# Kernel tuning notes

Hardware: AMD Instinct MI355X
Metric: run time of the kernel (lower is better)

The kernel has to match this reference:

```python
import jax, jax.numpy as jnp
import numpy as np

HIDDEN = 1024
HEADS = 16
HEAD_DIM = HIDDEN // HEADS


def setup_inputs() -> dict:
    key = jax.random.key(0)
    k1, k2, k3, k4 = jax.random.split(key, 4)
    x = jax.random.normal(k1, (4, 2048, HIDDEN), dtype=jnp.float32)
    # qkv: Linear(hidden, 3*hidden, bias=False) -> weight [3*hidden, hidden]
    w_qkv = jax.random.normal(k2, (3 * HIDDEN, HIDDEN), dtype=jnp.float32) * (HIDDEN ** -0.5)
    # out_proj: Linear(hidden, hidden) with bias
    w_out = jax.random.normal(k3, (HIDDEN, HIDDEN), dtype=jnp.float32) * (HIDDEN ** -0.5)
    b_out = jax.random.normal(k4, (HIDDEN,), dtype=jnp.float32) * 0.01
    return {"x": x, "w_qkv": w_qkv, "w_out": w_out, "b_out": b_out}


def reference(x, w_qkv, w_out, b_out):
    B, N, _ = x.shape
    scale = HEAD_DIM ** -0.5
    qkv = jnp.einsum('bnc,dc->bnd', x, w_qkv)            # [B,N,3*hidden]
    qkv = qkv.reshape(B, N, 3, HEADS, HEAD_DIM)
    qkv = jnp.transpose(qkv, (2, 0, 3, 1, 4))            # [3,B,H,N,hd]
    q, k, v = qkv[0], qkv[1], qkv[2]
    att = jnp.einsum('bhxd,bhyd->bhxy', q, k) * scale    # [B,H,N,N]
    att = jax.nn.softmax(att, axis=-1)
    out = jnp.einsum('bhxy,bhyd->bhxd', att, v)          # [B,H,N,hd]
    out = jnp.transpose(out, (0, 2, 1, 3)).reshape(B, N, HIDDEN)
    out = jnp.einsum('bnc,dc->bnd', out, w_out) + b_out
    return out
```

## Files before the change

kernel.cpp:

```cpp
#include <hip/hip_runtime.h>

typedef unsigned short u16;
typedef short short8 __attribute__((ext_vector_type(8)));
typedef float f32x4 __attribute__((ext_vector_type(4)));
typedef float f32x16 __attribute__((ext_vector_type(16)));
typedef unsigned short u16x4 __attribute__((ext_vector_type(4)));
typedef unsigned int u32x4 __attribute__((ext_vector_type(4)));

#define MFMA16(a, b, c) __builtin_amdgcn_mfma_f32_16x16x32_bf16((a), (b), (c), 0, 0, 0)
#define MFMA32(a, b, c) __builtin_amdgcn_mfma_f32_32x32x16_bf16((a), (b), (c), 0, 0, 0)

#if __has_builtin(__builtin_amdgcn_exp2f)
#define EXP2F(x) __builtin_amdgcn_exp2f(x)
#else
#define EXP2F(x) exp2f(x)
#endif

__device__ __forceinline__ u16 f2bf(float f) {
    unsigned u = __builtin_bit_cast(unsigned, f);
    u += 0x7FFFu + ((u >> 16) & 1u);
    return (u16)(u >> 16);
}

__device__ __forceinline__ void async16(void* lds, const void* g) {
    __builtin_amdgcn_global_load_lds(
        (const __attribute__((address_space(1))) void*)g,
        (__attribute__((address_space(3))) void*)lds, 16, 0, 0);
}

__device__ __forceinline__ unsigned cvtpk(float lo, float hi) {
    unsigned r;
    asm("v_cvt_pk_bf16_f32 %0, %1, %2" : "=v"(r) : "v"(lo), "v"(hi));
    return r;
}
__device__ __forceinline__ void plswap(unsigned& a, unsigned& b) {
    asm("v_permlane32_swap_b32 %0, %1" : "+v"(a), "+v"(b));
}

__device__ __forceinline__ void packP(const f32x16& s, short8& f0, short8& f1) {
    u32x4 u0, u1;
    {
        unsigned a = cvtpk(s[0], s[1]), b = cvtpk(s[4], s[5]);
        plswap(a, b);
        unsigned c = cvtpk(s[2], s[3]), d = cvtpk(s[6], s[7]);
        plswap(c, d);
        u0[0] = a; u0[1] = c; u0[2] = b; u0[3] = d;
    }
    {
        unsigned a = cvtpk(s[8], s[9]), b = cvtpk(s[12], s[13]);
        plswap(a, b);
        unsigned c = cvtpk(s[10], s[11]), d = cvtpk(s[14], s[15]);
        plswap(c, d);
        u1[0] = a; u1[1] = c; u1[2] = b; u1[3] = d;
    }
    f0 = __builtin_bit_cast(short8, u0);
    f1 = __builtin_bit_cast(short8, u1);
}

__global__ __launch_bounds__(256) void cast3(const float* __restrict__ x,
                                             const float* __restrict__ wqkv,
                                             const float* __restrict__ wout,
                                             u16* __restrict__ dst) {
    const int blk = blockIdx.x;
    const float* src;
    int idx;
    float sc = 1.0f;
    u16* out;
    if (blk < 8192) {
        src = x; out = dst; idx = (blk * 256 + threadIdx.x) * 4;
    } else if (blk < 11264) {
        src = wqkv; out = dst + (size_t)8192 * 1024;
        idx = ((blk - 8192) * 256 + threadIdx.x) * 4;
        if (idx < 1024 * 1024) sc = 0.18033688011112042f;
    } else {
        src = wout; out = dst + (size_t)11264 * 1024;
        idx = ((blk - 11264) * 256 + threadIdx.x) * 4;
    }
    float4 v = *(const float4*)(src + idx);
    u16x4 r;
    r[0] = f2bf(v.x * sc); r[1] = f2bf(v.y * sc);
    r[2] = f2bf(v.z * sc); r[3] = f2bf(v.w * sc);
    *(u16x4*)(out + idx) = r;
}

template <int MODE>
__global__ __launch_bounds__(256, 2) void gemm_bt(const u16* __restrict__ A,
                                                  const u16* __restrict__ B,
                                                  void* __restrict__ C0,
                                                  void* __restrict__ C1,
                                                  int M, int N, int K) {
    __shared__ u16 As[128 * 32];
    __shared__ u16 Bs[128 * 32];
    const int tid = threadIdx.x;
    const int w = tid >> 6, l = tid & 63;
    const int g = l >> 4, lo = l & 15;
    const int mtiles = M >> 7;
    const int tm = blockIdx.x % mtiles, tn = blockIdx.x / mtiles;
    const int rowBase = tm << 7, colBase = tn << 7;
    const int wrow = w >> 1, wcol = w & 1;

    f32x4 acc[4][4] = {};

    const int srow = l >> 2;
    const int scol = (l & 3) * 8;
    const int nk = K >> 5;
    for (int kt = 0; kt < nk; ++kt) {
        const int kbase = kt * 32 + scol;
#pragma unroll
        for (int it = 0; it < 2; ++it) {
            const int seg = it * 4 + w;
            const int r = seg * 16 + srow;
            async16(&As[seg * 512], &A[(size_t)(rowBase + r) * K + kbase]);
            async16(&Bs[seg * 512], &B[(size_t)(colBase + r) * K + kbase]);
        }
        __syncthreads();
        short8 af[4], bf[4];
#pragma unroll
        for (int mi = 0; mi < 4; ++mi)
            af[mi] = *(const short8*)&As[(wrow * 64 + mi * 16 + lo) * 32 + g * 8];
#pragma unroll
        for (int ni = 0; ni < 4; ++ni)
            bf[ni] = *(const short8*)&Bs[(wcol * 64 + ni * 16 + lo) * 32 + g * 8];
#pragma unroll
        for (int mi = 0; mi < 4; ++mi)
#pragma unroll
            for (int ni = 0; ni < 4; ++ni)
                acc[mi][ni] = MFMA16(af[mi], bf[ni], acc[mi][ni]);
        __syncthreads();
    }

    if constexpr (MODE == 0) {
        if (colBase < 2048) {
            u16* qk = (u16*)C0;
#pragma unroll
            for (int ni = 0; ni < 4; ++ni) {
                const int c = colBase + wcol * 64 + ni * 16 + lo;
#pragma unroll
                for (int mi = 0; mi < 4; ++mi) {
                    const int r0 = rowBase + wrow * 64 + mi * 16 + g * 4;
#pragma unroll
                    for (int i = 0; i < 4; ++i)
                        qk[(size_t)(r0 + i) * 2048 + c] = f2bf(acc[mi][ni][i]);
                }
            }
        } else {
            u16* vt = (u16*)C1;
            const int b = rowBase >> 11;
#pragma unroll
            for (int ni = 0; ni < 4; ++ni) {
                const int c = colBase + wcol * 64 + ni * 16 + lo;
                const int hh = (c - 2048) >> 6, d = (c - 2048) & 63;
                u16* vrow = vt + ((size_t)((b * 16 + hh) * 64 + d)) * 2048;
#pragma unroll
                for (int mi = 0; mi < 4; ++mi) {
                    const int r0 = rowBase + wrow * 64 + mi * 16 + g * 4;
                    u16x4 pk;
#pragma unroll
                    for (int i = 0; i < 4; ++i) pk[i] = f2bf(acc[mi][ni][i]);
                    *(u16x4*)(vrow + (r0 & 2047)) = pk;
                }
            }
        }
    } else {
        float* Cf = (float*)C0;
        const float* bias = (const float*)C1;
#pragma unroll
        for (int ni = 0; ni < 4; ++ni) {
            const int c = colBase + wcol * 64 + ni * 16 + lo;
            const float bv = bias[c];
#pragma unroll
            for (int mi = 0; mi < 4; ++mi) {
                const int r0 = rowBase + wrow * 64 + mi * 16 + g * 4;
#pragma unroll
                for (int i = 0; i < 4; ++i)
                    Cf[(size_t)(r0 + i) * N + c] = acc[mi][ni][i] + bv;
            }
        }
    }
}

__global__ __launch_bounds__(256, 4) void attn_fwd(const u16* __restrict__ qkb,
                                                   const u16* __restrict__ vtg,
                                                   u16* __restrict__ outb) {
    __shared__ u16 Ks[2][64 * 64];
    __shared__ u16 Vs[2][64 * 64];
    const int tid = threadIdx.x;
    const int w = tid >> 6, l = tid & 63;
    const int hi = l >> 5, lq = l & 31;

    const int lin = (blockIdx.x & 7) * 128 + (blockIdx.x >> 3);
    const int bh = lin >> 4, qt = lin & 15;
    const int b = bh >> 4, h = bh & 15;
    const size_t rowQ = (size_t)b * 2048 + qt * 128 + w * 32;

    short8 qf[4];
#pragma unroll
    for (int ks = 0; ks < 4; ++ks)
        qf[ks] = *(const short8*)(qkb + (rowQ + lq) * 2048 + h * 64 + ks * 16 + hi * 8);

    int koff[4];
#pragma unroll
    for (int ks = 0; ks < 4; ++ks)
        koff[ks] = (lq * 128 + ks * 32 + hi * 16) ^ ((lq & 7) << 4);

    const int L0 = tid * 16, L1 = tid * 16 + 4096;
    const int kr0 = L0 >> 7, kc0 = ((L0 ^ ((kr0 & 7) << 4)) & 127) >> 1;
    const int kr1 = L1 >> 7, kc1 = ((L1 ^ ((kr1 & 7) << 4)) & 127) >> 1;
    const u16* ks0 = qkb + (size_t)(b * 2048 + kr0) * 2048 + 1024 + h * 64 + kc0;
    const u16* ks1 = qkb + (size_t)(b * 2048 + kr1) * 2048 + 1024 + h * 64 + kc1;
    const u16* vs0 = vtg + ((size_t)bh * 64 + kr0) * 2048 + kc0;
    const u16* vs1 = vtg + ((size_t)bh * 64 + kr1) * 2048 + kc1;
    const size_t KADV = (size_t)64 * 2048;

    f32x16 O0, O1, Ol;
#pragma unroll
    for (int i = 0; i < 16; ++i) { O0[i] = 0.f; O1[i] = 0.f; Ol[i] = 0.f; }
    const f32x16 Z = {};
    const short8 onesv = {16256, 16256, 16256, 16256, 16256, 16256, 16256, 16256};

    async16((char*)Ks[0] + L0, ks0); async16((char*)Ks[0] + L1, ks1);
    async16((char*)Vs[0] + L0, vs0); async16((char*)Vs[0] + L1, vs1);
    ks0 += KADV; ks1 += KADV; vs0 += 64; vs1 += 64;

    int cur = 0;
    for (int kt = 0; kt < 32; ++kt) {
        __syncthreads();
        if (kt < 31) {
            const int nx = cur ^ 1;
            async16((char*)Ks[nx] + L0, ks0); async16((char*)Ks[nx] + L1, ks1);
            async16((char*)Vs[nx] + L0, vs0); async16((char*)Vs[nx] + L1, vs1);
            ks0 += KADV; ks1 += KADV; vs0 += 64; vs1 += 64;
        }
        const char* kb = (const char*)Ks[cur];
        const char* vb = (const char*)Vs[cur];

#pragma unroll
        for (int t = 0; t < 2; ++t) {
            const int tb = t * 4096;
            __builtin_amdgcn_s_setprio(1);
            f32x16 s = MFMA32(*(const short8*)(kb + koff[0] + tb), qf[0], Z);
            s = MFMA32(*(const short8*)(kb + koff[1] + tb), qf[1], s);
            s = MFMA32(*(const short8*)(kb + koff[2] + tb), qf[2], s);
            s = MFMA32(*(const short8*)(kb + koff[3] + tb), qf[3], s);
            __builtin_amdgcn_s_setprio(0);

#pragma unroll
            for (int i = 0; i < 16; ++i) s[i] = EXP2F(s[i]);

            short8 p0, p1;
            packP(s, p0, p1);

            __builtin_amdgcn_s_setprio(1);
            Ol = MFMA32(p0, onesv, Ol);
            Ol = MFMA32(p1, onesv, Ol);
            O0 = MFMA32(p0, *(const short8*)(vb + koff[t * 2]), O0);
            O1 = MFMA32(p0, *(const short8*)(vb + koff[t * 2] + 4096), O1);
            O0 = MFMA32(p1, *(const short8*)(vb + koff[t * 2 + 1]), O0);
            O1 = MFMA32(p1, *(const short8*)(vb + koff[t * 2 + 1] + 4096), O1);
            __builtin_amdgcn_s_setprio(0);
        }
        cur ^= 1;
    }

#pragma unroll
    for (int r = 0; r < 16; ++r) {
        const int qrow = (r & 3) + 8 * (r >> 2) + 4 * hi;
        const float linv = 1.0f / Ol[r];
        u16* op = outb + (rowQ + qrow) * 1024 + h * 64 + lq;
        op[0] = f2bf(O0[r] * linv);
        op[32] = f2bf(O1[r] * linv);
    }
}

extern "C" void kernel_launch(void* const* d_in, const int* in_sizes, int n_in,
                              void* d_out, int out_size, void* d_ws, size_t ws_size,
                              hipStream_t stream) {
    const float* x     = (const float*)d_in[0];
    const float* w_qkv = (const float*)d_in[1];
    const float* w_out = (const float*)d_in[2];
    const float* b_out = (const float*)d_in[3];
    float* out = (float*)d_out;

    u16* xb    = (u16*)d_ws;
    u16* wqkvb = xb    + (size_t)8192 * 1024;
    u16* woutb = wqkvb + (size_t)3072 * 1024;
    u16* qkb   = woutb + (size_t)1024 * 1024;
    u16* vtg   = qkb   + (size_t)8192 * 2048;
    u16* attb  = vtg   + (size_t)64 * 64 * 2048;

    cast3<<<12288, 256, 0, stream>>>(x, w_qkv, w_out, xb);

    gemm_bt<0><<<dim3((8192 / 128) * (3072 / 128)), 256, 0, stream>>>(
        xb, wqkvb, qkb, vtg, 8192, 3072, 1024);

    attn_fwd<<<1024, 256, 0, stream>>>(qkb, vtg, attb);

    gemm_bt<1><<<dim3((8192 / 128) * (1024 / 128)), 256, 0, stream>>>(
        attb, woutb, out, (void*)b_out, 8192, 1024, 1024);
}
```

Before: 187.9 us.

## Replace QKV projection GEMM with 256x256-tile double-buffered swizzled kernel

The QKV projection now runs in a new 512-thread kernel that computes 256x256 output tiles with a 64-wide K step. It double-buffers global-to-LDS async loads, uses an XOR-swizzled LDS layout to avoid bank conflicts, and raises wave priority around the MFMA bursts. The goal is more data reuse per loaded byte and overlap of loads with matrix math, replacing the 128x128, single-buffered, 32-wide-K kernel. In exchange it uses more registers and 128KB of LDS, and launches only 384 blocks, which may hurt occupancy and load balance. The output projection keeps the old kernel, now specialised to the bias mode only.

New measurement: 187.0 us. No clear change (-0.5%).

```diff
diff --git a/kernel.cpp b/kernel.cpp
--- a/kernel.cpp
+++ b/kernel.cpp
@@ -83,11 +83,127 @@
     *(u16x4*)(out + idx) = r;
 }
 
-template <int MODE>
+__global__ __launch_bounds__(512, 2) void gemm256(const u16* __restrict__ A,
+                                                  const u16* __restrict__ B,
+                                                  u16* __restrict__ qk,
+                                                  u16* __restrict__ vt) {
+    __shared__ u16 lds[2][2][16384];
+    const int tid = threadIdx.x;
+    const int l = tid & 63;
+    const int w = tid >> 6;
+    const int g = l >> 4, lo = l & 15;
+    const int wrow = w >> 2, wcol = w & 3;
+    const int tm = blockIdx.x & 31, tn = blockIdx.x >> 5;
+    const int rowBase = tm << 8, colBase = tn << 8;
+
+    const int srow = tid >> 3;
+    const int scol = (((tid * 16) ^ (((tid >> 3) & 7) << 4)) & 127) >> 1;
+    const u16* pa = A + (size_t)(rowBase + srow) * 1024 + scol;
+    const u16* pb = B + (size_t)(colBase + srow) * 1024 + scol;
+    const int ldsOff = tid * 16;
+
+    int abase[2], bbase[2];
+#pragma unroll
+    for (int k = 0; k < 2; ++k) {
+        abase[k] = (((wrow * 128 + lo) * 128 + k * 64 + g * 16) ^ ((lo & 7) << 4));
+        bbase[k] = (((wcol * 64 + lo) * 128 + k * 64 + g * 16) ^ ((lo & 7) << 4));
+    }
+
+    f32x4 acc[8][4] = {};
+
+#define STAGE256(buf, kt)                                                                   \
+    {                                                                                       \
+        const u16* sa = pa + (kt) * 64;                                                     \
+        const u16* sb = pb + (kt) * 64;                                                     \
+        _Pragma("unroll")                                                                   \
+        for (int i = 0; i < 4; ++i) {                                                       \
+            async16((char*)lds[buf][0] + ldsOff + i * 8192, sa + (size_t)i * 64 * 1024);    \
+            async16((char*)lds[buf][1] + ldsOff + i * 8192, sb + (size_t)i * 64 * 1024);    \
+        }                                                                                   \
+    }
+
+    STAGE256(0, 0);
+    __syncthreads();
+
+    for (int kt = 0; kt < 16; ++kt) {
+        const int cur = kt & 1;
+        if (kt < 15) STAGE256(cur ^ 1, kt + 1);
+        const char* la = (const char*)lds[cur][0];
+        const char* lb = (const char*)lds[cur][1];
+
+        short8 bf[4][2], af[4][2];
+#pragma unroll
+        for (int n = 0; n < 4; ++n)
+#pragma unroll
+            for (int k = 0; k < 2; ++k)
+                bf[n][k] = *(const short8*)(lb + bbase[k] + n * 2048);
+#pragma unroll
+        for (int m = 0; m < 4; ++m)
+#pragma unroll
+            for (int k = 0; k < 2; ++k)
+                af[m][k] = *(const short8*)(la + abase[k] + m * 2048);
+        __builtin_amdgcn_s_setprio(1);
+#pragma unroll
+        for (int m = 0; m < 4; ++m)
+#pragma unroll
+            for (int n = 0; n < 4; ++n) {
+                acc[m][n] = MFMA16(af[m][0], bf[n][0], acc[m][n]);
+                acc[m][n] = MFMA16(af[m][1], bf[n][1], acc[m][n]);
+            }
+        __builtin_amdgcn_s_setprio(0);
+#pragma unroll
+        for (int m = 0; m < 4; ++m)
+#pragma unroll
+            for (int k = 0; k < 2; ++k)
+                af[m][k] = *(const short8*)(la + abase[k] + (m + 4) * 2048);
+        __builtin_amdgcn_s_setprio(1);
+#pragma unroll
+        for (int m = 0; m < 4; ++m)
+#pragma unroll
+            for (int n = 0; n < 4; ++n) {
+                acc[m + 4][n] = MFMA16(af[m][0], bf[n][0], acc[m + 4][n]);
+                acc[m + 4][n] = MFMA16(af[m][1], bf[n][1], acc[m + 4][n]);
+            }
+        __builtin_amdgcn_s_setprio(0);
+        __syncthreads();
+    }
+#undef STAGE256
+
+    if (colBase < 2048) {
+#pragma unroll
+        for (int n = 0; n < 4; ++n) {
+            const int c = colBase + wcol * 64 + n * 16 + lo;
+#pragma unroll
+            for (int m = 0; m < 8; ++m) {
+                const int r0 = rowBase + wrow * 128 + m * 16 + g * 4;
+#pragma unroll
+                for (int i = 0; i < 4; ++i)
+                    qk[(size_t)(r0 + i) * 2048 + c] = f2bf(acc[m][n][i]);
+            }
+        }
+    } else {
+        const int b = rowBase >> 11;
+#pragma unroll
+        for (int n = 0; n < 4; ++n) {
+            const int c = colBase + wcol * 64 + n * 16 + lo;
+            const int hh = (c - 2048) >> 6, d = (c - 2048) & 63;
+            u16* vrow = vt + ((size_t)((b * 16 + hh) * 64 + d)) * 2048;
+#pragma unroll
+            for (int m = 0; m < 8; ++m) {
+                const int r0 = rowBase + wrow * 128 + m * 16 + g * 4;
+                u16x4 pk;
+#pragma unroll
+                for (int i = 0; i < 4; ++i) pk[i] = f2bf(acc[m][n][i]);
+                *(u16x4*)(vrow + (r0 & 2047)) = pk;
+            }
+        }
+    }
+}
+
 __global__ __launch_bounds__(256, 2) void gemm_bt(const u16* __restrict__ A,
                                                   const u16* __restrict__ B,
-                                                  void* __restrict__ C0,
-                                                  void* __restrict__ C1,
+                                                  float* __restrict__ Cf,
+                                                  const float* __restrict__ bias,
                                                   int M, int N, int K) {
     __shared__ u16 As[128 * 32];
     __shared__ u16 Bs[128 * 32];
@@ -129,52 +245,16 @@
         __syncthreads();
     }
 
-    if constexpr (MODE == 0) {
-        if (colBase < 2048) {
-            u16* qk = (u16*)C0;
-#pragma unroll
-            for (int ni = 0; ni < 4; ++ni) {
-                const int c = colBase + wcol * 64 + ni * 16 + lo;
-#pragma unroll
-                for (int mi = 0; mi < 4; ++mi) {
-                    const int r0 = rowBase + wrow * 64 + mi * 16 + g * 4;
-#pragma unroll
-                    for (int i = 0; i < 4; ++i)
-                        qk[(size_t)(r0 + i) * 2048 + c] = f2bf(acc[mi][ni][i]);
-                }
-            }
-        } else {
-            u16* vt = (u16*)C1;
-            const int b = rowBase >> 11;
-#pragma unroll
-            for (int ni = 0; ni < 4; ++ni) {
-                const int c = colBase + wcol * 64 + ni * 16 + lo;
-                const int hh = (c - 2048) >> 6, d = (c - 2048) & 63;
-                u16* vrow = vt + ((size_t)((b * 16 + hh) * 64 + d)) * 2048;
-#pragma unroll
-                for (int mi = 0; mi < 4; ++mi) {
-                    const int r0 = rowBase + wrow * 64 + mi * 16 + g * 4;
-                    u16x4 pk;
-#pragma unroll
-                    for (int i = 0; i < 4; ++i) pk[i] = f2bf(acc[mi][ni][i]);
-                    *(u16x4*)(vrow + (r0 & 2047)) = pk;
-                }
-            }
-        }
-    } else {
-        float* Cf = (float*)C0;
-        const float* bias = (const float*)C1;
-#pragma unroll
-        for (int ni = 0; ni < 4; ++ni) {
-            const int c = colBase + wcol * 64 + ni * 16 + lo;
-            const float bv = bias[c];
-#pragma unroll
-            for (int mi = 0; mi < 4; ++mi) {
-                const int r0 = rowBase + wrow * 64 + mi * 16 + g * 4;
-#pragma unroll
-                for (int i = 0; i < 4; ++i)
-                    Cf[(size_t)(r0 + i) * N + c] = acc[mi][ni][i] + bv;
-            }
+#pragma unroll
+    for (int ni = 0; ni < 4; ++ni) {
+        const int c = colBase + wcol * 64 + ni * 16 + lo;
+        const float bv = bias[c];
+#pragma unroll
+        for (int mi = 0; mi < 4; ++mi) {
+            const int r0 = rowBase + wrow * 64 + mi * 16 + g * 4;
+#pragma unroll
+            for (int i = 0; i < 4; ++i)
+                Cf[(size_t)(r0 + i) * N + c] = acc[mi][ni][i] + bv;
         }
     }
 }
@@ -290,11 +370,10 @@
 
     cast3<<<12288, 256, 0, stream>>>(x, w_qkv, w_out, xb);
 
-    gemm_bt<0><<<dim3((8192 / 128) * (3072 / 128)), 256, 0, stream>>>(
-        xb, wqkvb, qkb, vtg, 8192, 3072, 1024);
+    gemm256<<<384, 512, 0, stream>>>(xb, wqkvb, qkb, vtg);
 
     attn_fwd<<<1024, 256, 0, stream>>>(qkb, vtg, attb);
 
-    gemm_bt<1><<<dim3((8192 / 128) * (1024 / 128)), 256, 0, stream>>>(
-        attb, woutb, out, (void*)b_out, 8192, 1024, 1024);
-}
+    gemm_bt<<<dim3((8192 / 128) * (1024 / 128)), 256, 0, stream>>>(
+        attb, woutb, out, b_out, 8192, 1024, 1024);
+}
```
